# Optimization experiments

Measured on AMD Instinct MI355X. Metric: run time of the kernel, lower is better.

## Reference

```python
import math
import jax, jax.numpy as jnp
import numpy as np

N_HEADS = 16
D_EMBED = 1024

def setup_inputs() -> dict:
    key = jax.random.key(0)
    ks = jax.random.split(key, 5)
    b, l, d = 2, 2048, D_EMBED
    return {
        "x": jax.random.normal(ks[0], (b, l, d), dtype=jnp.float32),
        "w_in": jax.random.normal(ks[1], (3 * d, d), dtype=jnp.float32) * 0.02,
        "b_in": jax.random.normal(ks[2], (3 * d,), dtype=jnp.float32) * 0.02,
        "w_out": jax.random.normal(ks[3], (d, d), dtype=jnp.float32) * 0.02,
        "b_out": jax.random.normal(ks[4], (d,), dtype=jnp.float32) * 0.02,
    }

def reference(x, w_in, b_in, w_out, b_out):
    b, l, d = x.shape
    h = N_HEADS
    scale = 1.0 / math.sqrt(d // h)
    # in_proj then reshape to heads BEFORE chunking (faithful to source:
    # each head's 3*d_head block is split into q/k/v)
    x_proj = (x @ w_in.T + b_in).reshape(b, l, h, -1)  # (b,l,h,3*dh)
    q, k, v = jnp.split(x_proj, 3, axis=-1)            # each (b,l,h,dh)
    att = jnp.einsum('blhd,bmhd->blmh', q, k) * scale  # (b,l,m,h)
    # causal_mask=False path of the original forward
    att = jax.nn.softmax(att, axis=2)                  # softmax over keys m
    # faithful to source einsum 'blmh, blhd-> blhd' (sums att over m against
    # v indexed by l, exactly as the original code computes)
    opt = jnp.einsum('blmh,blhd->blhd', att, v).reshape(b, l, d)
    return opt @ w_out.T + b_out
```

## Files before the change

kernel.cpp:

```cpp
#include <hip/hip_runtime.h>

typedef unsigned short ushort_t;
typedef __bf16 bf16x8 __attribute__((ext_vector_type(8)));
typedef float f32x4 __attribute__((ext_vector_type(4)));

static __device__ __forceinline__ ushort_t f2bf(float f) {
    __bf16 b = (__bf16)f;
    return __builtin_bit_cast(ushort_t, b);
}

#define GLOAD_LDS16(gptr, lptr)                                                        \
    __builtin_amdgcn_global_load_lds(                                                  \
        (const __attribute__((address_space(1))) void*)(gptr),                         \
        (__attribute__((address_space(3))) void*)(lptr), 16, 0, 0)

#define CFENCE() asm volatile("" ::: "memory")
#define LGKM0_SCHED() do { asm volatile("s_waitcnt lgkmcnt(0)" ::: "memory");          \
                           __builtin_amdgcn_sched_barrier(0); } while (0)

template <int N> __device__ __forceinline__ void waitcnt_vm() {
    if constexpr (N == 0)       asm volatile("s_waitcnt vmcnt(0)" ::: "memory");
    else if constexpr (N == 4)  asm volatile("s_waitcnt vmcnt(4)" ::: "memory");
    else if constexpr (N == 8)  asm volatile("s_waitcnt vmcnt(8)" ::: "memory");
}

template <int BM, int BN, int WGM, int WGN, int THREADS, bool BF16_OUT>
__device__ __forceinline__
void gemm_core64(const ushort_t* __restrict__ A, const ushort_t* __restrict__ B,
                 const float* __restrict__ bias, void* __restrict__ C,
                 const int K, const int N, const int rA, const int rB,
                 ushort_t* ls) {
    constexpr int WM = BM / WGM, WN = BN / WGN;
    constexpr int MI = WM / 16, NJ = WN / 16;
    constexpr int LA = (BM * 8) / THREADS;
    constexpr int LB = (BN * 8) / THREADS;
    constexpr int L  = LA + LB;
    constexpr int HALF = (BM + BN) * 64;

    const int tid  = threadIdx.x;
    const int lane = tid & 63;
    const int wv   = tid >> 6;
    const int wr   = wv / WGN, wc = wv % WGN;
    const int fr   = lane & 15, fq = lane >> 4;

    f32x4 acc[MI][NJ] = {};

    auto stage = [&](int k0, int buf) {
        #pragma unroll
        for (int q = 0; q < LA; ++q) {
            int c = q * THREADS + tid;
            int row = c >> 3;
            int u = (c & 7) ^ (row & 7);
            GLOAD_LDS16(A + (size_t)(rA + row) * K + k0 + u * 8,
                        &ls[buf * HALF + c * 8]);
        }
        #pragma unroll
        for (int q = 0; q < LB; ++q) {
            int c = q * THREADS + tid;
            int row = c >> 3;
            int u = (c & 7) ^ (row & 7);
            GLOAD_LDS16(B + (size_t)(rB + row) * K + k0 + u * 8,
                        &ls[buf * HALF + BM * 64 + c * 8]);
        }
    };

    auto compute = [&](int buf) {
        #pragma unroll
        for (int sub = 0; sub < 2; ++sub) {
            const int u = sub * 4 + fq;
            bf16x8 af[MI], bfv[NJ];
            #pragma unroll
            for (int i = 0; i < MI; ++i) {
                const int row = wr * WM + i * 16 + fr;
                af[i] = *(const bf16x8*)&ls[buf * HALF + row * 64 + (u ^ (row & 7)) * 8];
            }
            #pragma unroll
            for (int j = 0; j < NJ; ++j) {
                const int row = wc * WN + j * 16 + fr;
                bfv[j] = *(const bf16x8*)&ls[buf * HALF + BM * 64 + row * 64 + (u ^ (row & 7)) * 8];
            }
            #pragma unroll
            for (int i = 0; i < MI; ++i)
                #pragma unroll
                for (int j = 0; j < NJ; ++j)
                    acc[i][j] = __builtin_amdgcn_mfma_f32_16x16x32_bf16(af[i], bfv[j], acc[i][j], 0, 0, 0);
        }
    };

    const int T = K >> 6;
    stage(0, 0);
    stage(64, 1);
    int cur = 0, nxt2 = 2;
    for (int t = 0; t < T - 2; ++t) {
        stage((t + 2) << 6, nxt2);
        waitcnt_vm<2 * L>();
        __builtin_amdgcn_s_barrier(); CFENCE();
        compute(cur);
        LGKM0_SCHED();
        __builtin_amdgcn_s_barrier(); CFENCE();
        cur  = (cur  + 1 == 3) ? 0 : cur  + 1;
        nxt2 = (nxt2 + 1 == 3) ? 0 : nxt2 + 1;
    }
    waitcnt_vm<L>();
    __builtin_amdgcn_s_barrier(); CFENCE();
    compute(cur);
    cur = (cur + 1 == 3) ? 0 : cur + 1;
    LGKM0_SCHED();
    waitcnt_vm<0>();
    __builtin_amdgcn_s_barrier(); CFENCE();
    compute(cur);

    const int orow0 = rA + wr * WM + fq * 4;
    const int ocol0 = rB + wc * WN + fr;
    #pragma unroll
    for (int i = 0; i < MI; ++i)
        #pragma unroll
        for (int j = 0; j < NJ; ++j) {
            const int col = ocol0 + j * 16;
            const float bv = bias ? bias[col] : 0.f;
            #pragma unroll
            for (int r = 0; r < 4; ++r) {
                const int row = orow0 + i * 16 + r;
                const float v = acc[i][j][r] + bv;
                if constexpr (BF16_OUT)
                    ((ushort_t*)C)[(size_t)row * N + col] = f2bf(v);
                else
                    ((float*)C)[(size_t)row * N + col] = v;
            }
        }
}

__global__ __launch_bounds__(256)
void prep(const float* __restrict__ w_in, const float* __restrict__ w_out,
          ushort_t* __restrict__ wob, ushort_t* __restrict__ Pt) {
    __shared__ ushort_t tile[64][65];
    const int b = blockIdx.x;
    const int t = threadIdx.x;

    if (b < 128) {
        #pragma unroll
        for (int p = 0; p < 8; ++p) {
            int i = b * 2048 + p * 256 + t;
            float4 v = ((const float4*)w_out)[i];
            ushort4 o; o.x = f2bf(v.x); o.y = f2bf(v.y); o.z = f2bf(v.z); o.w = f2bf(v.w);
            ((ushort4*)wob)[i] = o;
        }
    } else {
        const int g = b - 128;
        const int gx = g & 15, gy = g >> 4;
        #pragma unroll
        for (int p = 0; p < 16; ++p) {
            int e = p * 256 + t;
            int j = e >> 6, c = e & 63;
            tile[j][c] = f2bf(w_in[(size_t)(gx * 192 + 128 + j) * 1024 + gy * 64 + c]);
        }
        __syncthreads();
        #pragma unroll
        for (int p = 0; p < 16; ++p) {
            int e = p * 256 + t;
            int c = e >> 6, j = e & 63;
            Pt[(size_t)(gy * 64 + c) * 1024 + gx * 64 + j] = tile[j][c];
        }
    }
}

__global__ __launch_bounds__(256)
void k2(const ushort_t* __restrict__ wob, const ushort_t* __restrict__ Pt,
        ushort_t* __restrict__ Wfb, const float* __restrict__ x,
        ushort_t* __restrict__ xb, const float* __restrict__ w_out,
        const float* __restrict__ b_in, const float* __restrict__ b_out,
        float* __restrict__ bfused) {
    __shared__ alignas(16) ushort_t ls[3 * (64 + 64) * 64];
    const int b = blockIdx.x;
    const int t = threadIdx.x;
    if (b < 256) {
        const int swz = (b & 7) * 32 + (b >> 3);
        const int by = swz >> 4, bx = swz & 15;
        gemm_core64<64, 64, 2, 2, 256, true>(wob, Pt, nullptr, (void*)Wfb, 1024, 1024,
                                             by * 64, bx * 64, ls);
    } else if (b < 768) {
        const int g = b - 256;
        #pragma unroll
        for (int p = 0; p < 8; ++p) {
            int i = g * 2048 + p * 256 + t;
            float4 v = ((const float4*)x)[i];
            ushort4 o; o.x = f2bf(v.x); o.y = f2bf(v.y); o.z = f2bf(v.z); o.w = f2bf(v.w);
            ((ushort4*)xb)[i] = o;
        }
    } else {
        const int w = t >> 6, lane = t & 63;
        const int row = (b - 768) * 4 + w;
        float s = 0.f;
        #pragma unroll
        for (int it = 0; it < 16; ++it) {
            int j = it * 64 + lane;
            int r = (j >> 6) * 192 + 128 + (j & 63);
            s += w_out[(size_t)row * 1024 + j] * b_in[r];
        }
        #pragma unroll
        for (int off = 32; off; off >>= 1) s += __shfl_down(s, off, 64);
        if (lane == 0) bfused[row] = s + b_out[row];
    }
}

__global__ __launch_bounds__(512)
void k3(const ushort_t* __restrict__ xb, const ushort_t* __restrict__ Wfb,
        const float* __restrict__ bfused, float* __restrict__ out) {
    __shared__ alignas(16) ushort_t ls[3 * (128 + 128) * 64];
    const int b = blockIdx.x;
    const int swz = (b & 7) * 32 + (b >> 3);
    const int by = swz >> 3, bx = swz & 7;
    gemm_core64<128, 128, 2, 4, 512, false>(xb, Wfb, bfused, (void*)out, 1024, 1024,
                                            by * 128, bx * 128, ls);
}

extern "C" void kernel_launch(void* const* d_in, const int* in_sizes, int n_in,
                              void* d_out, int out_size, void* d_ws, size_t ws_size,
                              hipStream_t stream) {
    const float* x     = (const float*)d_in[0];
    const float* w_in  = (const float*)d_in[1];
    const float* b_in  = (const float*)d_in[2];
    const float* w_out = (const float*)d_in[3];
    const float* b_out = (const float*)d_in[4];
    float* out = (float*)d_out;

    char* ws = (char*)d_ws;
    ushort_t* xb     = (ushort_t*)(ws);
    ushort_t* wob    = (ushort_t*)(ws + (8u  << 20));
    ushort_t* Pt     = (ushort_t*)(ws + (10u << 20));
    ushort_t* Wfb    = (ushort_t*)(ws + (12u << 20));
    float*    bfused = (float*)   (ws + (14u << 20));

    prep<<<384, 256, 0, stream>>>(w_in, w_out, wob, Pt);
    k2<<<1024, 256, 0, stream>>>(wob, Pt, Wfb, x, xb, w_out, b_in, b_out, bfused);
    k3<<<256, 512, 0, stream>>>(xb, Wfb, bfused, out);
}
```

Before: 33.70 us.

## Fuse fp32-to-bf16 conversion of x into final GEMM A-operand load

The final GEMM now reads fp32 x directly, converts it to bf16 in registers and writes it into swizzled LDS, so the separate x conversion pass and its round trip through global memory go away. The fused-bias computation moves into the prep kernel, and k2 keeps only the weight-fusion GEMM. k3 gets its own double-buffered pipeline with register prefetch for A and direct-to-LDS loads for B, plus launch bounds of 512 threads with a minimum of 4 blocks per CU. In exchange, k3 reads twice as many bytes for A (fp32 instead of bf16) and spends VALU time converting inside the main loop.

Measured after the change: 37.12 us. 10.1% more time.

```diff
diff --git a/kernel.cpp b/kernel.cpp
--- a/kernel.cpp
+++ b/kernel.cpp
@@ -3,6 +3,7 @@
 typedef unsigned short ushort_t;
 typedef __bf16 bf16x8 __attribute__((ext_vector_type(8)));
 typedef float f32x4 __attribute__((ext_vector_type(4)));
+typedef ushort_t ushort8 __attribute__((ext_vector_type(8)));
 
 static __device__ __forceinline__ ushort_t f2bf(float f) {
     __bf16 b = (__bf16)f;
@@ -132,7 +133,9 @@
 
 __global__ __launch_bounds__(256)
 void prep(const float* __restrict__ w_in, const float* __restrict__ w_out,
-          ushort_t* __restrict__ wob, ushort_t* __restrict__ Pt) {
+          const float* __restrict__ b_in, const float* __restrict__ b_out,
+          ushort_t* __restrict__ wob, ushort_t* __restrict__ Pt,
+          float* __restrict__ bfused) {
     __shared__ ushort_t tile[64][65];
     const int b = blockIdx.x;
     const int t = threadIdx.x;
@@ -145,7 +148,7 @@
             ushort4 o; o.x = f2bf(v.x); o.y = f2bf(v.y); o.z = f2bf(v.z); o.w = f2bf(v.w);
             ((ushort4*)wob)[i] = o;
         }
-    } else {
+    } else if (b < 384) {
         const int g = b - 128;
         const int gx = g & 15, gy = g >> 4;
         #pragma unroll
@@ -161,35 +164,9 @@
             int c = e >> 6, j = e & 63;
             Pt[(size_t)(gy * 64 + c) * 1024 + gx * 64 + j] = tile[j][c];
         }
-    }
-}
-
-__global__ __launch_bounds__(256)
-void k2(const ushort_t* __restrict__ wob, const ushort_t* __restrict__ Pt,
-        ushort_t* __restrict__ Wfb, const float* __restrict__ x,
-        ushort_t* __restrict__ xb, const float* __restrict__ w_out,
-        const float* __restrict__ b_in, const float* __restrict__ b_out,
-        float* __restrict__ bfused) {
-    __shared__ alignas(16) ushort_t ls[3 * (64 + 64) * 64];
-    const int b = blockIdx.x;
-    const int t = threadIdx.x;
-    if (b < 256) {
-        const int swz = (b & 7) * 32 + (b >> 3);
-        const int by = swz >> 4, bx = swz & 15;
-        gemm_core64<64, 64, 2, 2, 256, true>(wob, Pt, nullptr, (void*)Wfb, 1024, 1024,
-                                             by * 64, bx * 64, ls);
-    } else if (b < 768) {
-        const int g = b - 256;
-        #pragma unroll
-        for (int p = 0; p < 8; ++p) {
-            int i = g * 2048 + p * 256 + t;
-            float4 v = ((const float4*)x)[i];
-            ushort4 o; o.x = f2bf(v.x); o.y = f2bf(v.y); o.z = f2bf(v.z); o.w = f2bf(v.w);
-            ((ushort4*)xb)[i] = o;
-        }
     } else {
         const int w = t >> 6, lane = t & 63;
-        const int row = (b - 768) * 4 + w;
+        const int row = (b - 384) * 4 + w;
         float s = 0.f;
         #pragma unroll
         for (int it = 0; it < 16; ++it) {
@@ -203,15 +180,121 @@
     }
 }
 
-__global__ __launch_bounds__(512)
-void k3(const ushort_t* __restrict__ xb, const ushort_t* __restrict__ Wfb,
+__global__ __launch_bounds__(256)
+void k2(const ushort_t* __restrict__ wob, const ushort_t* __restrict__ Pt,
+        ushort_t* __restrict__ Wfb) {
+    __shared__ alignas(16) ushort_t ls[3 * (64 + 64) * 64];
+    const int b = blockIdx.x;
+    const int swz = (b & 7) * 32 + (b >> 3);
+    const int by = swz >> 4, bx = swz & 15;
+    gemm_core64<64, 64, 2, 2, 256, true>(wob, Pt, nullptr, (void*)Wfb, 1024, 1024,
+                                         by * 64, bx * 64, ls);
+}
+
+__global__ __launch_bounds__(512, 4)
+void k3(const float* __restrict__ x, const ushort_t* __restrict__ Wfb,
         const float* __restrict__ bfused, float* __restrict__ out) {
-    __shared__ alignas(16) ushort_t ls[3 * (128 + 128) * 64];
+    constexpr int HALF = 16384;
+    __shared__ alignas(16) ushort_t ls[2 * HALF];
     const int b = blockIdx.x;
     const int swz = (b & 7) * 32 + (b >> 3);
     const int by = swz >> 3, bx = swz & 7;
-    gemm_core64<128, 128, 2, 4, 512, false>(xb, Wfb, bfused, (void*)out, 1024, 1024,
-                                            by * 128, bx * 128, ls);
+    const int rA = by * 128, rB = bx * 128;
+
+    const int tid  = threadIdx.x;
+    const int lane = tid & 63;
+    const int wv   = tid >> 6;
+    const int wr   = wv >> 2, wc = wv & 3;
+    const int fr   = lane & 15, fq = lane >> 4;
+
+    float4 rg[4];
+    auto aload = [&](int k0) {
+        #pragma unroll
+        for (int q = 0; q < 2; ++q) {
+            int c = q * 512 + tid; int row = c >> 3; int u = (c & 7) ^ (row & 7);
+            const float* p = x + (size_t)(rA + row) * 1024 + k0 + u * 8;
+            rg[q * 2 + 0] = ((const float4*)p)[0];
+            rg[q * 2 + 1] = ((const float4*)p)[1];
+        }
+    };
+    auto awrite = [&](int buf) {
+        #pragma unroll
+        for (int q = 0; q < 2; ++q) {
+            int c = q * 512 + tid;
+            const float4 v0 = rg[q * 2], v1 = rg[q * 2 + 1];
+            ushort8 o;
+            o[0]=f2bf(v0.x); o[1]=f2bf(v0.y); o[2]=f2bf(v0.z); o[3]=f2bf(v0.w);
+            o[4]=f2bf(v1.x); o[5]=f2bf(v1.y); o[6]=f2bf(v1.z); o[7]=f2bf(v1.w);
+            *(ushort8*)&ls[buf * HALF + c * 8] = o;
+        }
+    };
+    auto bstage = [&](int k0, int buf) {
+        #pragma unroll
+        for (int q = 0; q < 2; ++q) {
+            int c = q * 512 + tid; int row = c >> 3; int u = (c & 7) ^ (row & 7);
+            GLOAD_LDS16(Wfb + (size_t)(rB + row) * 1024 + k0 + u * 8,
+                        &ls[buf * HALF + 8192 + c * 8]);
+        }
+    };
+
+    f32x4 acc[4][2] = {};
+    auto compute = [&](int buf) {
+        #pragma unroll
+        for (int sub = 0; sub < 2; ++sub) {
+            const int u = sub * 4 + fq;
+            bf16x8 af[4], bfv[2];
+            #pragma unroll
+            for (int i = 0; i < 4; ++i) {
+                const int row = wr * 64 + i * 16 + fr;
+                af[i] = *(const bf16x8*)&ls[buf * HALF + row * 64 + (u ^ (row & 7)) * 8];
+            }
+            #pragma unroll
+            for (int j = 0; j < 2; ++j) {
+                const int row = wc * 32 + j * 16 + fr;
+                bfv[j] = *(const bf16x8*)&ls[buf * HALF + 8192 + row * 64 + (u ^ (row & 7)) * 8];
+            }
+            #pragma unroll
+            for (int i = 0; i < 4; ++i)
+                #pragma unroll
+                for (int j = 0; j < 2; ++j)
+                    acc[i][j] = __builtin_amdgcn_mfma_f32_16x16x32_bf16(af[i], bfv[j], acc[i][j], 0, 0, 0);
+        }
+    };
+
+    aload(0);
+    bstage(0, 0);
+    awrite(0);
+    LGKM0_SCHED();
+    waitcnt_vm<0>();
+    __builtin_amdgcn_s_barrier(); CFENCE();
+
+    for (int t = 0; t < 16; ++t) {
+        const int cur = t & 1;
+        if (t < 15) {
+            aload((t + 1) << 6);
+            bstage((t + 1) << 6, cur ^ 1);
+        }
+        compute(cur);
+        if (t < 15) {
+            awrite(cur ^ 1);
+            LGKM0_SCHED();
+            waitcnt_vm<0>();
+            __builtin_amdgcn_s_barrier(); CFENCE();
+        }
+    }
+
+    const int orow0 = rA + wr * 64 + fq * 4;
+    const int ocol0 = rB + wc * 32 + fr;
+    #pragma unroll
+    for (int i = 0; i < 4; ++i)
+        #pragma unroll
+        for (int j = 0; j < 2; ++j) {
+            const int col = ocol0 + j * 16;
+            const float bv = bfused[col];
+            #pragma unroll
+            for (int r = 0; r < 4; ++r)
+                out[(size_t)(orow0 + i * 16 + r) * 1024 + col] = acc[i][j][r] + bv;
+        }
 }
 
 extern "C" void kernel_launch(void* const* d_in, const int* in_sizes, int n_in,
@@ -225,13 +308,12 @@
     float* out = (float*)d_out;
 
     char* ws = (char*)d_ws;
-    ushort_t* xb     = (ushort_t*)(ws);
-    ushort_t* wob    = (ushort_t*)(ws + (8u  << 20));
-    ushort_t* Pt     = (ushort_t*)(ws + (10u << 20));
-    ushort_t* Wfb    = (ushort_t*)(ws + (12u << 20));
-    float*    bfused = (float*)   (ws + (14u << 20));
-
-    prep<<<384, 256, 0, stream>>>(w_in, w_out, wob, Pt);
-    k2<<<1024, 256, 0, stream>>>(wob, Pt, Wfb, x, xb, w_out, b_in, b_out, bfused);
-    k3<<<256, 512, 0, stream>>>(xb, Wfb, bfused, out);
-}
+    ushort_t* wob    = (ushort_t*)(ws);
+    ushort_t* Pt     = (ushort_t*)(ws + (2u << 20));
+    ushort_t* Wfb    = (ushort_t*)(ws + (4u << 20));
+    float*    bfused = (float*)   (ws + (6u << 20));
+
+    prep<<<640, 256, 0, stream>>>(w_in, w_out, b_in, b_out, wob, Pt, bfused);
+    k2<<<256, 256, 0, stream>>>(wob, Pt, Wfb);
+    k3<<<256, 512, 0, stream>>>(x, Wfb, bfused, out);
+}
```
